# Optimization experiments

Hardware: AMD Instinct MI355X
Metric: run time of the kernel (lower is better)

## Reference

```python
import jax, jax.numpy as jnp
import numpy as np

E = 16          # num_experts
D_FULL = 1024   # full_feature_dim
DM = 128        # expert_dim
S = D_FULL // E # per-expert feature slice = 64
P = 2048        # num patches
B = 8
C = 256
W = 3           # local_window (neighbor experts)
DEPTH = 8       # cantor_depth
NEG = -1e9


def _cantor_coord(pos, max_len, depth):
    x = pos / max(1, max_len - 1)
    x = max(1e-6, min(x, 1.0 - 1e-6))
    val, factor = 0.0, 0.5
    for _ in range(depth):
        x *= 3.0
        d = int(x)
        x -= d
        if d == 2:
            val += factor
        factor *= 0.5
    return val


def _expert_routes():
    coords = np.array([_cantor_coord(i, E, DEPTH) for i in range(E)], dtype=np.float32)
    return np.stack([np.argsort(np.abs(coords - coords[i]), kind='stable')[:W] for i in range(E)]).astype(np.int32)


ROUTES = _expert_routes()  # [E, W] static routing table


def setup_inputs():
    key = jax.random.key(0)
    ks = jax.random.split(key, 8)
    h = S // 4
    lim = float(np.sqrt(6.0 / (S + DM)))  # xavier_uniform bound
    penta = jax.random.normal(ks[5], (E, 5, DM), jnp.float32) * 0.02
    penta = penta / jnp.linalg.norm(penta, axis=-1, keepdims=True)
    return {
        'tokens': jax.random.normal(ks[0], (B, P, D_FULL), jnp.float32),
        'fingerprints': jax.random.uniform(ks[1], (P,), jnp.float32),
        'alpha': jnp.ones((E,), jnp.float32),
        'gate_w1': jax.random.normal(ks[2], (E, S, h), jnp.float32) * 0.05,
        'gate_b1': jnp.zeros((E, h), jnp.float32),
        'gate_w2': jax.random.normal(ks[3], (E, h, 1), jnp.float32) * 0.05,
        'gate_b2': jnp.zeros((E, 1), jnp.float32),
        'q_w': jax.random.uniform(ks[4], (E, S, DM), jnp.float32, -lim, lim),
        'k_w': jax.random.uniform(ks[6], (E, S, DM), jnp.float32, -lim, lim),
        'v_w': jax.random.uniform(ks[7], (E, S, DM), jnp.float32, -lim, lim),
        'penta': penta,
        'fusion_w': jnp.ones((5,), jnp.float32) / 5.0,
        'temperature': jnp.float32(0.5),
    }


def _dispatch(fingerprints):
    # Fingerprint band masks, then fixed-capacity gather (static shapes for jit).
    masks = []
    for e in range(E):
        lo, hi = e / E, (e + 1) / E
        m = (fingerprints >= lo) & ((fingerprints <= hi) if e == E - 1 else (fingerprints < hi))
        masks.append(m)
    masks = jnp.stack(masks)                             # [E, P]
    order = jnp.argsort(jnp.where(masks, 0, 1), axis=1)  # stable: assigned patches first
    idx = order[:, :C]                                   # [E, C]
    valid = jnp.take_along_axis(masks, idx, axis=1)      # [E, C]
    return idx, valid


def _forward(tokens, fingerprints, alpha, gate_w1, gate_b1, gate_w2, gate_b2,
             q_w, k_w, v_w, penta, fusion_w, temperature):
    idx, valid = _dispatch(fingerprints)
    Kaff, Qaff, Vs = [], [], []
    for e in range(E):  # fixed structural loop over experts
        feats = tokens[:, idx[e], e * S:(e + 1) * S]                       # [B, C, S]
        g = jax.nn.sigmoid(jax.nn.gelu(feats @ gate_w1[e] + gate_b1[e]) @ gate_w2[e] + gate_b2[e])
        aw = jax.nn.sigmoid(alpha[e])
        feats = feats * (g * aw + (1.0 - aw))                              # gated features
        Q = feats @ q_w[e]
        K = feats @ k_w[e]
        V = feats @ v_w[e]                                                 # [B, C, DM]
        dirs = penta[e] / jnp.linalg.norm(penta[e], axis=-1, keepdims=True)  # [5, DM]
        Kaff.append(jnp.einsum('bcd,vd->vbc', K, dirs))
        Qaff.append(jnp.einsum('bcd,vd->vbc', Q, dirs))
        Vs.append(V)
    Kaff = jnp.stack(Kaff)   # [E, 5, B, C]
    Qaff = jnp.stack(Qaff)   # [E, 5, B, C]
    Vs = jnp.stack(Vs)       # [E, B, C, DM]
    wdir = jax.nn.softmax(fusion_w)
    vmask = valid.astype(jnp.float32)
    out = jnp.zeros((B, P, DM), jnp.float32)
    for e in range(E):
        nb = ROUTES[e]                                  # static [W]
        Knb, Vnb, vnb = Kaff[nb], Vs[nb], vmask[nb]     # [W,5,B,C], [W,B,C,DM], [W,C]
        scores = jnp.einsum('vbi,nvbj->vbinj', Qaff[e], Knb) / temperature
        scores = jnp.where(vnb[None, None, None, :, :] > 0, scores, NEG)
        attn = jax.nn.softmax(scores.reshape(5, B, C, W * C), axis=-1).reshape(5, B, C, W, C)
        att = jnp.einsum('vbinj,nbjd->vbid', attn, Vnb)  # per-direction attended values
        out_e = jnp.einsum('v,vbid->bid', wdir, att) * vmask[e][None, :, None]
        out = out.at[:, idx[e]].add(out_e)              # scatter back to patch positions
    return out


def reference(tokens, fingerprints, alpha, gate_w1, gate_b1, gate_w2, gate_b2,
              q_w, k_w, v_w, penta, fusion_w, temperature):
    return _forward(tokens, fingerprints, alpha, gate_w1, gate_b1, gate_w2, gate_b2,
                    q_w, k_w, v_w, penta, fusion_w, temperature)
```

## Files before the change

kernel.cpp:

```cpp
#include <hip/hip_runtime.h>
#include <cfloat>
#include <math.h>

#define E 16
#define DFULL 1024
#define DM 128
#define S 64
#define P 2048
#define B 8
#define C 256
#define W 3
#define H 16
#define RQ 16
#define NCH 16
#define LOG2E 1.4426950408889634f
#define WST 272

typedef __attribute__((ext_vector_type(8))) short short8;
typedef __attribute__((ext_vector_type(4))) short short4v;
typedef __attribute__((ext_vector_type(4))) float f32x4;
#define MFMA_BF16(a, b, c) __builtin_amdgcn_mfma_f32_16x16x32_bf16((a), (b), (c), 0, 0, 0)

#if defined(__HIP_DEVICE_COMPILE__) && __has_builtin(__builtin_amdgcn_exp2f)
#define EXP2(x) __builtin_amdgcn_exp2f(x)
#else
#define EXP2(x) exp2f(x)
#endif

struct RoutesArg { int nb[E][W]; };

static void compute_routes(int r[E][W]) {
  float coords[E];
  for (int i = 0; i < E; ++i) {
    double x = (double)i / (double)(E - 1);
    if (x < 1e-06) x = 1e-06;
    if (x > 1.0 - 1e-06) x = 1.0 - 1e-06;
    double val = 0.0, factor = 0.5;
    for (int k = 0; k < 8; ++k) {
      x *= 3.0;
      int d = (int)x;
      x -= (double)d;
      if (d == 2) val += factor;
      factor *= 0.5;
    }
    coords[i] = (float)val;
  }
  for (int e = 0; e < E; ++e) {
    float de[E];
    for (int i = 0; i < E; ++i) de[i] = fabsf(coords[i] - coords[e]);
    bool used[E] = {false};
    for (int w = 0; w < W; ++w) {
      int best = -1; float bd = FLT_MAX;
      for (int i = 0; i < E; ++i)
        if (!used[i] && de[i] < bd) { bd = de[i]; best = i; }
      used[best] = true;
      r[e][w] = best;
    }
  }
}

__device__ __forceinline__ unsigned short bfhi(float x) {
  return (unsigned short)(__float_as_uint(x) >> 16);
}
__device__ __forceinline__ float bf2f(unsigned short h) {
  return __uint_as_float(((unsigned)h) << 16);
}
__device__ __forceinline__ float gelu_tanh(float x) {
  float u = 0.7978845608028654f * (x + 0.044715f * x * x * x);
  float ez = __expf(2.0f * u);
  float th = 1.0f - __fdividef(2.0f, ez + 1.0f);
  return 0.5f * x * (1.0f + th);
}
__device__ __forceinline__ float sigmoidf_(float x) {
  return __fdividef(1.0f, 1.0f + __expf(-x));
}

__global__ __launch_bounds__(256) void k_setup(
    const float* __restrict__ fp, const float* __restrict__ qw,
    const float* __restrict__ kw, const float* __restrict__ penta,
    const float* __restrict__ temp, const float* __restrict__ vw,
    int* __restrict__ idx, int* __restrict__ counts,
    unsigned short* __restrict__ qkdT_h, unsigned short* __restrict__ qkdT_l,
    unsigned short* __restrict__ vwT_h, unsigned short* __restrict__ vwT_l) {
  int e = blockIdx.x, t = threadIdx.x;
  __shared__ float s_tr[DM * 65];
  if (blockIdx.y == 1) {
    const float* vwe = vw + (size_t)e * S * DM;
    for (int u = t; u < S * DM; u += 256) {
      int s = u >> 7, d = u & 127;
      s_tr[d * 65 + s] = vwe[u];
    }
    __syncthreads();
    for (int u = t; u < S * DM; u += 256) {
      int d = u >> 6, s = u & 63;
      float f = s_tr[d * 65 + s];
      unsigned short h = bfhi(f), l = bfhi(f - bf2f(h));
      vwT_h[(size_t)e * 8192 + u] = h;
      vwT_l[(size_t)e * 8192 + u] = l;
    }
    return;
  }
  {
    float lo = (float)e * 0.0625f, hi = (float)(e + 1) * 0.0625f;
    bool last = (e == E - 1);
    int p0 = t * 8;
    int m[8]; int ls = 0;
    #pragma unroll
    for (int k = 0; k < 8; ++k) {
      float f = fp[p0 + k];
      bool mm = (f >= lo) && (last ? (f <= hi) : (f < hi));
      m[k] = mm ? 1 : 0;
      ls += m[k];
    }
    __shared__ int sc[256];
    sc[t] = ls;
    __syncthreads();
    for (int o = 1; o < 256; o <<= 1) {
      int v = (t >= o) ? sc[t - o] : 0;
      __syncthreads();
      sc[t] += v;
      __syncthreads();
    }
    int incl = sc[t];
    int M = sc[255];
    int r = incl - ls;
    #pragma unroll
    for (int k = 0; k < 8; ++k) {
      if (m[k]) {
        if (r < C) idx[e * C + r] = p0 + k;
        r++;
      }
    }
    if (t == 0) counts[e] = (M < C) ? M : C;
  }
  __syncthreads();
  __shared__ float s_rn[5];
  if (t < 5) {
    const float* pv = penta + (e * 5 + t) * DM;
    float ss = 0.f;
    for (int d = 0; d < DM; ++d) ss += pv[d] * pv[d];
    s_rn[t] = 1.0f / sqrtf(ss);
  }
  __syncthreads();
  float invT = 1.0f / temp[0];
  int s = t & 63, cg = t >> 6;
  for (int c = cg; c < 10; c += 4) {
    int v = c % 5;
    bool isq = (c < 5);
    const float* wrow = (isq ? qw : kw) + ((size_t)e * S + s) * DM;
    const float* pv = penta + (e * 5 + v) * DM;
    float acc = 0.f;
    #pragma unroll
    for (int d4 = 0; d4 < DM / 4; ++d4) {
      float4 a = ((const float4*)wrow)[d4];
      float4 p = ((const float4*)pv)[d4];
      acc += a.x * p.x + a.y * p.y + a.z * p.z + a.w * p.w;
    }
    float val = acc * s_rn[v] * (isq ? invT : 1.0f);
    unsigned short h = bfhi(val), l = bfhi(val - bf2f(h));
    qkdT_h[(e * 16 + c) * 64 + s] = h;
    qkdT_l[(e * 16 + c) * 64 + s] = l;
  }
  for (int c = 10 + cg; c < 16; c += 4) {
    qkdT_h[(e * 16 + c) * 64 + s] = 0;
    qkdT_l[(e * 16 + c) * 64 + s] = 0;
  }
}

__global__ __launch_bounds__(512, 8) void k_p1(
    const float* __restrict__ tokens, const float* __restrict__ alpha,
    const float* __restrict__ gw1, const float* __restrict__ gb1,
    const float* __restrict__ gw2, const float* __restrict__ gb2,
    const unsigned short* __restrict__ qkdT_h, const unsigned short* __restrict__ qkdT_l,
    const unsigned short* __restrict__ vwT_h, const unsigned short* __restrict__ vwT_l,
    const int* __restrict__ idx, const int* __restrict__ counts,
    float* __restrict__ Qa, float* __restrict__ Ka,
    unsigned short* __restrict__ Vt_h, unsigned short* __restrict__ Vt_l,
    float* __restrict__ kmx, float* __restrict__ kmn,
    float* __restrict__ out) {
  int e = blockIdx.x, b = blockIdx.y, rq = blockIdx.z;
  int t = threadIdx.x;

  {
    int blk = (e * B + b) * NCH + rq;
    if (t < 256) {
      float4 z4 = {0.f, 0.f, 0.f, 0.f};
      ((float4*)out)[(size_t)blk * 256 + t] = z4;
    }
  }

  int Me = counts[e];
  int r0 = rq * RQ;
  if (r0 >= Me) {
    if (t < 5) {
      kmx[((e * 5 + t) * B + b) * NCH + rq] = -FLT_MAX;
      kmn[((e * 5 + t) * B + b) * NCH + rq] = FLT_MAX;
    }
    return;
  }

  __shared__ float s_f[RQ * 65];
  __shared__ __align__(16) unsigned short s_fh[RQ * 72];
  __shared__ __align__(16) unsigned short s_fl[RQ * 72];
  __shared__ float s_gw1[S * H];
  __shared__ float s_gh[RQ * 8 * H];
  __shared__ float s_scl[RQ];
  __shared__ float s_kx[5 * RQ], s_kn[5 * RQ];
  __shared__ __align__(16) unsigned short s_vth[DM * 16];
  __shared__ __align__(16) unsigned short s_vtl[DM * 16];

  if (t < 256) {
    int row = t >> 4, q4 = t & 15;
    int ii = r0 + row;
    int pos = (ii < Me) ? idx[e * C + ii] : idx[e * C];
    const float* trow = tokens + ((size_t)b * P + pos) * DFULL + e * S;
    float4 v4 = ((const float4*)trow)[q4];
    s_f[row * 65 + q4 * 4 + 0] = v4.x;
    s_f[row * 65 + q4 * 4 + 1] = v4.y;
    s_f[row * 65 + q4 * 4 + 2] = v4.z;
    s_f[row * 65 + q4 * 4 + 3] = v4.w;
    ((float4*)s_gw1)[t] = ((const float4*)(gw1 + (size_t)e * S * H))[t];
  }
  __syncthreads();

  if (t < 128) {
    int row = t >> 3, sq = t & 7;
    float hh[H];
    #pragma unroll
    for (int j = 0; j < H; ++j) hh[j] = 0.f;
    #pragma unroll
    for (int k = 0; k < 8; ++k) {
      int s = sq * 8 + k;
      float fs = s_f[row * 65 + s];
      const float* gr = s_gw1 + s * H;
      #pragma unroll
      for (int j = 0; j < H; ++j) hh[j] += fs * gr[j];
    }
    #pragma unroll
    for (int j = 0; j < H; ++j) s_gh[(row * 8 + sq) * H + j] = hh[j];
  }
  __syncthreads();
  if (t < RQ) {
    float z = gb2[e];
    #pragma unroll
    for (int j = 0; j < H; ++j) {
      float hj = gb1[e * H + j];
      #pragma unroll
      for (int p = 0; p < 8; ++p) hj += s_gh[(t * 8 + p) * H + j];
      z += gelu_tanh(hj) * gw2[e * H + j];
    }
    float aw = sigmoidf_(alpha[e]);
    s_scl[t] = sigmoidf_(z) * aw + (1.0f - aw);
  }
  __syncthreads();
  if (t < 256) {
    int row = t >> 4, s0 = (t & 15) * 4;
    float sc = s_scl[row];
    #pragma unroll
    for (int k = 0; k < 4; ++k) {
      float f = s_f[row * 65 + s0 + k] * sc;
      unsigned short h = bfhi(f), l = bfhi(f - bf2f(h));
      s_fh[row * 72 + s0 + k] = h;
      s_fl[row * 72 + s0 + k] = l;
    }
  }
  __syncthreads();

  int L = t & 63, wv = t >> 6, quad = L >> 4, col = L & 15;

  {
    const unsigned short* vTh = vwT_h + (size_t)e * 8192;
    const unsigned short* vTl = vwT_l + (size_t)e * 8192;
    f32x4 va = {0.f, 0.f, 0.f, 0.f};
    int d0 = wv * 16 + col;
    #pragma unroll
    for (int kc = 0; kc < 2; ++kc) {
      int ko = kc * 32 + quad * 8;
      short8 ah = *(const short8*)(s_fh + col * 72 + ko);
      short8 al = *(const short8*)(s_fl + col * 72 + ko);
      short8 bh = *(const short8*)(vTh + d0 * 64 + ko);
      short8 bl = *(const short8*)(vTl + d0 * 64 + ko);
      va = MFMA_BF16(ah, bh, va);
      va = MFMA_BF16(ah, bl, va);
      va = MFMA_BF16(al, bh, va);
    }
    #pragma unroll
    for (int reg = 0; reg < 4; ++reg) {
      int row = quad * 4 + reg;
      float f0 = va[reg];
      unsigned short h0 = bfhi(f0), l0 = bfhi(f0 - bf2f(h0));
      s_vth[d0 * 16 + row] = h0;
      s_vtl[d0 * 16 + row] = l0;
    }
  }

  if (wv == 0) {
    const unsigned short* qTh = qkdT_h + e * 16 * 64;
    const unsigned short* qTl = qkdT_l + e * 16 * 64;
    f32x4 qa = {0.f, 0.f, 0.f, 0.f};
    #pragma unroll
    for (int kc = 0; kc < 2; ++kc) {
      int ko = kc * 32 + quad * 8;
      short8 ah = *(const short8*)(s_fh + col * 72 + ko);
      short8 al = *(const short8*)(s_fl + col * 72 + ko);
      short8 bh = *(const short8*)(qTh + col * 64 + ko);
      short8 bl = *(const short8*)(qTl + col * 64 + ko);
      qa = MFMA_BF16(ah, bh, qa);
      qa = MFMA_BF16(ah, bl, qa);
      qa = MFMA_BF16(al, bh, qa);
    }
    #pragma unroll
    for (int reg = 0; reg < 4; ++reg) {
      int row = quad * 4 + reg;
      int ii = r0 + row;
      float val = qa[reg];
      if (col < 5) {
        if (ii < Me) Qa[((e * 5 + col) * B + b) * C + ii] = val;
      } else if (col < 10) {
        int v = col - 5;
        if (ii < Me) Ka[((e * 5 + v) * B + b) * C + ii] = val;
        s_kx[v * RQ + row] = (ii < Me) ? val : -FLT_MAX;
        s_kn[v * RQ + row] = (ii < Me) ? val : FLT_MAX;
      }
    }
  }
  __syncthreads();
  if (t < 5) {
    float mx = -FLT_MAX, mn = FLT_MAX;
    for (int r = 0; r < RQ; ++r) {
      mx = fmaxf(mx, s_kx[t * RQ + r]);
      mn = fminf(mn, s_kn[t * RQ + r]);
    }
    kmx[((e * 5 + t) * B + b) * NCH + rq] = mx;
    kmn[((e * 5 + t) * B + b) * NCH + rq] = mn;
  }
  if (t < 256) {
    size_t base = (size_t)(e * B + b) * (DM * C);
    int jsl = t >> 7, d = t & 127;
    size_t dst = base + ((size_t)(rq * 2 + jsl) * DM + d) * 8;
    int src = d * 16 + jsl * 8;
    *(short8*)(Vt_h + dst) = *(const short8*)(s_vth + src);
    *(short8*)(Vt_l + dst) = *(const short8*)(s_vtl + src);
  }
}

__global__ __launch_bounds__(512, 8) void k_p2v(
    const float* __restrict__ Qa, const float* __restrict__ Ka,
    const unsigned short* __restrict__ Vt_h, const unsigned short* __restrict__ Vt_l,
    const float* __restrict__ kmx, const float* __restrict__ kmn,
    const int* __restrict__ idx, const int* __restrict__ counts,
    const float* __restrict__ fusw, float* __restrict__ out, RoutesArg R) {
  int e = blockIdx.x, b = blockIdx.y, rq = blockIdx.z;
  int t = threadIdx.x;
  int Me = counts[e];
  int r0 = rq * RQ;
  if (r0 >= Me) return;

  __shared__ __align__(16) float s_ka[3 * 5 * C];
  __shared__ __align__(16) unsigned short s_wh[RQ * WST];
  __shared__ __align__(16) unsigned short s_wl[RQ * WST];
  __shared__ float s_lp[8 * 5 * RQ];
  __shared__ float s_KX[5], s_KN[5];
  __shared__ float s_l[5 * RQ];

  int nbs[3] = {R.nb[e][0], R.nb[e][1], R.nb[e][2]};
  int Mns[3] = {counts[nbs[0]], counts[nbs[1]], counts[nbs[2]]};
  int row = t & 15, jq = t >> 4;
  int ii = r0 + row;
  int L = t & 63, wv = t >> 6, quad = L >> 4, col = L & 15;

  for (int u = t; u < 960; u += 512) {
    int n = (u >= 640) ? 2 : ((u >= 320) ? 1 : 0);
    int r2 = u - n * 320;
    int v = r2 >> 6, off = r2 & 63;
    ((float4*)s_ka)[n * 320 + (v << 6) + off] =
        ((const float4*)(Ka + (((size_t)nbs[n] * 5 + v) * B + b) * C))[off];
  }
  if (wv < 5) {
    float KX = -FLT_MAX, KN = FLT_MAX;
    if (L < 48) {
      int n = L >> 4, k = L & 15;
      int base = ((nbs[n] * 5 + wv) * B + b) * NCH + k;
      KX = kmx[base];
      KN = kmn[base];
    }
    #pragma unroll
    for (int off = 32; off; off >>= 1) {
      KX = fmaxf(KX, __shfl_xor(KX, off));
      KN = fminf(KN, __shfl_xor(KN, off));
    }
    if (L == 0) { s_KX[wv] = KX; s_KN[wv] = KN; }
  }
  __syncthreads();

  float q2[5], m2[5];
  #pragma unroll
  for (int v = 0; v < 5; ++v) {
    float qv = Qa[(((size_t)e * 5 + v) * B + b) * C + ii];
    q2[v] = qv * LOG2E;
    m2[v] = ((qv > 0.f) ? qv * s_KX[v] : qv * s_KN[v]) * LOG2E;
  }

  float lp[5] = {0.f, 0.f, 0.f, 0.f, 0.f};
  for (int n = 0; n < 3; ++n) {
    const float* ka_n = s_ka + n * 1280;
    int Mn = Mns[n];
    for (int j = jq; j < Mn; j += 32) {
      #pragma unroll
      for (int v = 0; v < 5; ++v)
        lp[v] += EXP2(fmaf(q2[v], ka_n[v * C + j], -m2[v]));
    }
  }
  #pragma unroll
  for (int v = 0; v < 5; ++v) {
    lp[v] += __shfl_xor(lp[v], 16);
    lp[v] += __shfl_xor(lp[v], 32);
  }
  if (L < 16) {
    #pragma unroll
    for (int v = 0; v < 5; ++v) s_lp[(wv * 5 + v) * RQ + L] = lp[v];
  }
  __syncthreads();
  if (t < 80) {
    int v = t >> 4, rw = t & 15;
    float l = 0.f;
    #pragma unroll
    for (int w = 0; w < 8; ++w) l += s_lp[(w * 5 + v) * RQ + rw];
    s_l[v * RQ + rw] = l;
  }
  __syncthreads();

  float fw[5];
  #pragma unroll
  for (int v = 0; v < 5; ++v) fw[v] = fusw[v];
  float fmx = fw[0];
  #pragma unroll
  for (int v = 1; v < 5; ++v) fmx = fmaxf(fmx, fw[v]);
  float fsum = 0.f;
  #pragma unroll
  for (int v = 0; v < 5; ++v) { fw[v] = __expf(fw[v] - fmx); fsum += fw[v]; }
  float rfs = __fdividef(1.0f, fsum);
  float c2[5];
  #pragma unroll
  for (int v = 0; v < 5; ++v) {
    float cl = __fdividef(fw[v] * rfs, s_l[v * RQ + row]);
    c2[v] = __log2f(cl) - m2[v];
  }

  int d0 = wv * 16 + col;
  f32x4 acc = {0.f, 0.f, 0.f, 0.f};

  for (int n = 0; n < 3; ++n) {
    int ne = nbs[n], Mn = Mns[n];
    int kcN = (Mn + 31) >> 5;
    const float* ka_n = s_ka + n * 1280;
    __syncthreads();
    int jlim = kcN * 32;
    for (int j0 = jq * 4; j0 < jlim; j0 += 128) {
      short4v h4, l4;
      #pragma unroll
      for (int k2 = 0; k2 < 4; ++k2) {
        int jj = j0 + k2;
        float ww = 0.f;
        if (jj < Mn) {
          #pragma unroll
          for (int v = 0; v < 5; ++v)
            ww += EXP2(fmaf(q2[v], ka_n[v * C + jj], c2[v]));
        }
        unsigned short h = bfhi(ww), l = bfhi(ww - bf2f(h));
        h4[k2] = (short)h;
        l4[k2] = (short)l;
      }
      *(short4v*)(s_wh + row * WST + j0) = h4;
      *(short4v*)(s_wl + row * WST + j0) = l4;
    }
    __syncthreads();
    const unsigned short* vbh = Vt_h + (size_t)(ne * B + b) * (DM * C);
    const unsigned short* vbl = Vt_l + (size_t)(ne * B + b) * (DM * C);
    size_t sb0 = ((size_t)quad * DM + d0) * 8;
    short8 bh = *(const short8*)(vbh + sb0);
    short8 bl = *(const short8*)(vbl + sb0);
    for (int kc = 0; kc < kcN; ++kc) {
      int kn = (kc + 1 < kcN) ? (kc + 1) : kc;
      size_t sb = ((size_t)(kn * 4 + quad) * DM + d0) * 8;
      short8 nbh = *(const short8*)(vbh + sb);
      short8 nbl = *(const short8*)(vbl + sb);
      int ko = kc * 32 + quad * 8;
      short8 ah = *(const short8*)(s_wh + col * WST + ko);
      short8 al = *(const short8*)(s_wl + col * WST + ko);
      acc = MFMA_BF16(ah, bh, acc);
      acc = MFMA_BF16(ah, bl, acc);
      acc = MFMA_BF16(al, bh, acc);
      bh = nbh;
      bl = nbl;
    }
  }

  #pragma unroll
  for (int reg = 0; reg < 4; ++reg) {
    int rr = quad * 4 + reg;
    int iw = r0 + rr;
    if (iw < Me) {
      int pos = idx[e * C + iw];
      out[((size_t)b * P + pos) * DM + d0] = acc[reg];
    }
  }
}

extern "C" void kernel_launch(void* const* d_in, const int* in_sizes, int n_in,
                              void* d_out, int out_size, void* d_ws, size_t ws_size,
                              hipStream_t stream) {
  const float* tokens = (const float*)d_in[0];
  const float* fingerprints = (const float*)d_in[1];
  const float* alpha = (const float*)d_in[2];
  const float* gw1 = (const float*)d_in[3];
  const float* gb1 = (const float*)d_in[4];
  const float* gw2 = (const float*)d_in[5];
  const float* gb2 = (const float*)d_in[6];
  const float* qw = (const float*)d_in[7];
  const float* kw = (const float*)d_in[8];
  const float* vw = (const float*)d_in[9];
  const float* penta = (const float*)d_in[10];
  const float* fusw = (const float*)d_in[11];
  const float* temp = (const float*)d_in[12];
  float* out = (float*)d_out;

  float* ws = (float*)d_ws;
  float* Qa = ws;
  float* Ka = Qa + (size_t)E * 5 * B * C;
  float* kmx = Ka + (size_t)E * 5 * B * C;
  float* kmn = kmx + (size_t)E * 5 * B * NCH;
  unsigned short* qkdT_h = (unsigned short*)(kmn + (size_t)E * 5 * B * NCH);
  unsigned short* qkdT_l = qkdT_h + (size_t)E * 16 * 64;
  unsigned short* vwT_h = qkdT_l + (size_t)E * 16 * 64;
  unsigned short* vwT_l = vwT_h + (size_t)E * S * DM;
  unsigned short* Vt_h = vwT_l + (size_t)E * S * DM;
  unsigned short* Vt_l = Vt_h + (size_t)E * B * DM * C;
  int* idx = (int*)(Vt_l + (size_t)E * B * DM * C);
  int* counts = idx + (size_t)E * C;

  RoutesArg R;
  compute_routes(R.nb);

  k_setup<<<dim3(E, 2), dim3(256), 0, stream>>>(fingerprints, qw, kw, penta, temp, vw,
                                                idx, counts, qkdT_h, qkdT_l, vwT_h, vwT_l);
  k_p1<<<dim3(E, B, NCH), dim3(512), 0, stream>>>(tokens, alpha, gw1, gb1, gw2, gb2,
                                                  qkdT_h, qkdT_l, vwT_h, vwT_l,
                                                  idx, counts, Qa, Ka, Vt_h, Vt_l,
                                                  kmx, kmn, out);
  k_p2v<<<dim3(E, B, NCH), dim3(512), 0, stream>>>(Qa, Ka, Vt_h, Vt_l, kmx, kmn,
                                                   idx, counts, fusw, out, R);
}
```

Measured before the change: 177.2 us.

## Parallelize gate reduction, hoist loads, alias LDS, and raise MFMA loop priority

In k_p1, the gate second stage moves from 16 threads looping over 16 hidden units to 256 threads with a shuffle reduction, and s_gh is padded to stride 17 to avoid LDS bank conflicts. In k_p2v, the Qa and fusion-weight global loads are moved ahead of the Ka staging so their latency overlaps it. s_lp now reuses the s_wh buffer to cut LDS use, and the first V-fragment loads are issued before the weight-build phase. The MFMA loop also runs at raised wave priority via s_setprio, which could affect scheduling among co-resident waves.

Measured after the change: 172.9 us. -2.4%, faster.

```diff
diff --git a/kernel.cpp b/kernel.cpp
--- a/kernel.cpp
+++ b/kernel.cpp
@@ -13,6 +13,8 @@
 #define H 16
 #define RQ 16
 #define NCH 16
+#define RQ2 16
+#define NCH2 16
 #define LOG2E 1.4426950408889634f
 #define WST 272
 
@@ -203,7 +205,7 @@
   __shared__ __align__(16) unsigned short s_fh[RQ * 72];
   __shared__ __align__(16) unsigned short s_fl[RQ * 72];
   __shared__ float s_gw1[S * H];
-  __shared__ float s_gh[RQ * 8 * H];
+  __shared__ float s_gh[RQ * 8 * 17];
   __shared__ float s_scl[RQ];
   __shared__ float s_kx[5 * RQ], s_kn[5 * RQ];
   __shared__ __align__(16) unsigned short s_vth[DM * 16];
@@ -237,20 +239,21 @@
       for (int j = 0; j < H; ++j) hh[j] += fs * gr[j];
     }
     #pragma unroll
-    for (int j = 0; j < H; ++j) s_gh[(row * 8 + sq) * H + j] = hh[j];
-  }
-  __syncthreads();
-  if (t < RQ) {
-    float z = gb2[e];
-    #pragma unroll
-    for (int j = 0; j < H; ++j) {
-      float hj = gb1[e * H + j];
-      #pragma unroll
-      for (int p = 0; p < 8; ++p) hj += s_gh[(t * 8 + p) * H + j];
-      z += gelu_tanh(hj) * gw2[e * H + j];
-    }
-    float aw = sigmoidf_(alpha[e]);
-    s_scl[t] = sigmoidf_(z) * aw + (1.0f - aw);
+    for (int j = 0; j < H; ++j) s_gh[(row * 8 + sq) * 17 + j] = hh[j];
+  }
+  __syncthreads();
+  if (t < 256) {
+    int row = t >> 4, j = t & 15;
+    float hj = gb1[e * H + j];
+    #pragma unroll
+    for (int p = 0; p < 8; ++p) hj += s_gh[(row * 8 + p) * 17 + j];
+    float gz = gelu_tanh(hj) * gw2[e * H + j];
+    #pragma unroll
+    for (int off = 1; off < 16; off <<= 1) gz += __shfl_xor(gz, off);
+    if (j == 0) {
+      float aw = sigmoidf_(alpha[e]);
+      s_scl[row] = sigmoidf_(gb2[e] + gz) * aw + (1.0f - aw);
+    }
   }
   __syncthreads();
   if (t < 256) {
@@ -353,21 +356,29 @@
   int e = blockIdx.x, b = blockIdx.y, rq = blockIdx.z;
   int t = threadIdx.x;
   int Me = counts[e];
-  int r0 = rq * RQ;
+  int r0 = rq * RQ2;
   if (r0 >= Me) return;
 
   __shared__ __align__(16) float s_ka[3 * 5 * C];
-  __shared__ __align__(16) unsigned short s_wh[RQ * WST];
-  __shared__ __align__(16) unsigned short s_wl[RQ * WST];
-  __shared__ float s_lp[8 * 5 * RQ];
+  __shared__ __align__(16) unsigned short s_wh[RQ2 * WST];
+  __shared__ __align__(16) unsigned short s_wl[RQ2 * WST];
+  __shared__ float s_l[5 * RQ2];
   __shared__ float s_KX[5], s_KN[5];
-  __shared__ float s_l[5 * RQ];
+  float* s_lp = (float*)s_wh;
 
   int nbs[3] = {R.nb[e][0], R.nb[e][1], R.nb[e][2]};
   int Mns[3] = {counts[nbs[0]], counts[nbs[1]], counts[nbs[2]]};
   int row = t & 15, jq = t >> 4;
   int ii = r0 + row;
   int L = t & 63, wv = t >> 6, quad = L >> 4, col = L & 15;
+
+  float qv[5];
+  #pragma unroll
+  for (int v = 0; v < 5; ++v)
+    qv[v] = Qa[(((size_t)e * 5 + v) * B + b) * C + ii];
+  float fw[5];
+  #pragma unroll
+  for (int v = 0; v < 5; ++v) fw[v] = fusw[v];
 
   for (int u = t; u < 960; u += 512) {
     int n = (u >= 640) ? 2 : ((u >= 320) ? 1 : 0);
@@ -396,9 +407,8 @@
   float q2[5], m2[5];
   #pragma unroll
   for (int v = 0; v < 5; ++v) {
-    float qv = Qa[(((size_t)e * 5 + v) * B + b) * C + ii];
-    q2[v] = qv * LOG2E;
-    m2[v] = ((qv > 0.f) ? qv * s_KX[v] : qv * s_KN[v]) * LOG2E;
+    q2[v] = qv[v] * LOG2E;
+    m2[v] = ((qv[v] > 0.f) ? qv[v] * s_KX[v] : qv[v] * s_KN[v]) * LOG2E;
   }
 
   float lp[5] = {0.f, 0.f, 0.f, 0.f, 0.f};
@@ -418,21 +428,18 @@
   }
   if (L < 16) {
     #pragma unroll
-    for (int v = 0; v < 5; ++v) s_lp[(wv * 5 + v) * RQ + L] = lp[v];
+    for (int v = 0; v < 5; ++v) s_lp[(wv * 5 + v) * RQ2 + L] = lp[v];
   }
   __syncthreads();
   if (t < 80) {
     int v = t >> 4, rw = t & 15;
     float l = 0.f;
     #pragma unroll
-    for (int w = 0; w < 8; ++w) l += s_lp[(w * 5 + v) * RQ + rw];
-    s_l[v * RQ + rw] = l;
-  }
-  __syncthreads();
-
-  float fw[5];
-  #pragma unroll
-  for (int v = 0; v < 5; ++v) fw[v] = fusw[v];
+    for (int w = 0; w < 8; ++w) l += s_lp[(w * 5 + v) * RQ2 + rw];
+    s_l[v * RQ2 + rw] = l;
+  }
+  __syncthreads();
+
   float fmx = fw[0];
   #pragma unroll
   for (int v = 1; v < 5; ++v) fmx = fmaxf(fmx, fw[v]);
@@ -443,7 +450,7 @@
   float c2[5];
   #pragma unroll
   for (int v = 0; v < 5; ++v) {
-    float cl = __fdividef(fw[v] * rfs, s_l[v * RQ + row]);
+    float cl = __fdividef(fw[v] * rfs, s_l[v * RQ2 + row]);
     c2[v] = __log2f(cl) - m2[v];
   }
 
@@ -455,6 +462,11 @@
     int kcN = (Mn + 31) >> 5;
     const float* ka_n = s_ka + n * 1280;
     __syncthreads();
+    const unsigned short* vbh = Vt_h + (size_t)(ne * B + b) * (DM * C);
+    const unsigned short* vbl = Vt_l + (size_t)(ne * B + b) * (DM * C);
+    size_t sb0 = ((size_t)quad * DM + d0) * 8;
+    short8 bh = *(const short8*)(vbh + sb0);
+    short8 bl = *(const short8*)(vbl + sb0);
     int jlim = kcN * 32;
     for (int j0 = jq * 4; j0 < jlim; j0 += 128) {
       short4v h4, l4;
@@ -475,11 +487,7 @@
       *(short4v*)(s_wl + row * WST + j0) = l4;
     }
     __syncthreads();
-    const unsigned short* vbh = Vt_h + (size_t)(ne * B + b) * (DM * C);
-    const unsigned short* vbl = Vt_l + (size_t)(ne * B + b) * (DM * C);
-    size_t sb0 = ((size_t)quad * DM + d0) * 8;
-    short8 bh = *(const short8*)(vbh + sb0);
-    short8 bl = *(const short8*)(vbl + sb0);
+    __builtin_amdgcn_s_setprio(1);
     for (int kc = 0; kc < kcN; ++kc) {
       int kn = (kc + 1 < kcN) ? (kc + 1) : kc;
       size_t sb = ((size_t)(kn * 4 + quad) * DM + d0) * 8;
@@ -494,6 +502,7 @@
       bh = nbh;
       bl = nbl;
     }
+    __builtin_amdgcn_s_setprio(0);
   }
 
   #pragma unroll
@@ -548,6 +557,6 @@
                                                   qkdT_h, qkdT_l, vwT_h, vwT_l,
                                                   idx, counts, Qa, Ka, Vt_h, Vt_l,
                                                   kmx, kmn, out);
-  k_p2v<<<dim3(E, B, NCH), dim3(512), 0, stream>>>(Qa, Ka, Vt_h, Vt_l, kmx, kmn,
-                                                   idx, counts, fusw, out, R);
-}
+  k_p2v<<<dim3(E, B, NCH2), dim3(512), 0, stream>>>(Qa, Ka, Vt_h, Vt_l, kmx, kmn,
+                                                    idx, counts, fusw, out, R);
+}
```
